# Kernel tuning notes

Hardware: AMD Instinct MI355X
Metric: run time of the kernel (lower is better)

## Reference

```python
import jax, jax.numpy as jnp
import numpy as np

HEADS = 8
K = 3            # kernel_size per axis
RPB = 2 * K - 1  # rel-pos-bias extent per axis
EPS = 1e-5


def _nbr(dim, k):
    # NATTEN-style clamped window: shift window to stay fully inside [0, dim)
    q = jnp.arange(dim)
    start = jnp.clip(q - k // 2, 0, dim - k)
    nbr = start[:, None] + jnp.arange(k)[None, :]       # (dim, k) neighbor coords
    rel = nbr - q[:, None] + (k - 1)                    # (dim, k) in [0, 2k-2]
    return nbr, rel


def _instance_norm(x):
    # InstanceNorm3d, affine=False: normalize over spatial dims per (B, C)
    m = jnp.mean(x, axis=(2, 3, 4), keepdims=True)
    v = jnp.var(x, axis=(2, 3, 4), keepdims=True)
    return (x - m) * jax.lax.rsqrt(v + EPS)


def setup_inputs() -> dict:
    key = jax.random.key(0)
    ks = jax.random.split(key, 10)
    B, C, H, W, Z = 1, 128, 32, 32, 32
    Cf = 4 * C
    s = 0.02
    return {
        "x": jax.random.normal(ks[0], (B, C, H, W, Z), jnp.float32),
        "w_qkv": jax.random.normal(ks[1], (3 * C, C), jnp.float32) * s,
        "b_qkv": jnp.zeros((3 * C,), jnp.float32),
        "rpb": jax.random.normal(ks[2], (HEADS, RPB, RPB, RPB), jnp.float32) * s,
        "w_proj": jax.random.normal(ks[3], (C, C), jnp.float32) * s,
        "b_proj": jnp.zeros((C,), jnp.float32),
        "w_ffn1": jax.random.normal(ks[4], (Cf, C), jnp.float32) * s,
        "b_ffn1": jnp.zeros((Cf,), jnp.float32),
        "w_ffn2": jax.random.normal(ks[5], (C, Cf), jnp.float32) * s,
        "b_ffn2": jnp.zeros((C,), jnp.float32),
    }


def reference(x, w_qkv, b_qkv, rpb, w_proj, b_proj, w_ffn1, b_ffn1, w_ffn2, b_ffn2):
    B, C, H, W, Z = x.shape
    hd = C // HEADS
    N = H * W * Z
    KK = K ** 3

    # ---- SAM: 3D neighborhood self-attention ----
    xt = x.reshape(B, C, N).transpose(0, 2, 1)                 # (B, N, C)
    qkv = xt @ w_qkv.T + b_qkv                                  # (B, N, 3C)
    q, k_, v = jnp.split(qkv, 3, axis=-1)
    split = lambda t: t.reshape(B, N, HEADS, hd).transpose(0, 2, 1, 3)  # (B, h, N, d)
    q, k_, v = split(q), split(k_), split(v)

    nh, rh = _nbr(H, K)
    nw, rw = _nbr(W, K)
    nz, rz = _nbr(Z, K)
    # flat neighbor token index per (h, w, z, kh, kw, kz)
    nbr = ((nh[:, None, None, :, None, None] * W
            + nw[None, :, None, None, :, None]) * Z
           + nz[None, None, :, None, None, :]).reshape(N, KK)   # (N, 27)
    # flat rel-pos-bias index
    bidx = ((rh[:, None, None, :, None, None] * RPB
             + rw[None, :, None, None, :, None]) * RPB
            + rz[None, None, :, None, None, :]).reshape(N, KK)  # (N, 27)

    kg = k_[:, :, nbr]                                          # (B, h, N, 27, d)
    vg = v[:, :, nbr]                                           # (B, h, N, 27, d)
    bias = rpb.reshape(HEADS, RPB ** 3)[:, bidx]                # (h, N, 27)

    scale = jnp.asarray(hd, x.dtype) ** -0.5
    attn = jnp.einsum('bhnd,bhnkd->bhnk', q * scale, kg) + bias
    attn = jax.nn.softmax(attn, axis=-1)
    out = jnp.einsum('bhnk,bhnkd->bhnd', attn, vg)              # (B, h, N, d)
    out = out.transpose(0, 2, 1, 3).reshape(B, N, C) @ w_proj.T + b_proj
    x5 = out.transpose(0, 2, 1).reshape(B, C, H, W, Z)

    # ---- norm_in ----
    x5 = _instance_norm(x5)

    # ---- FFN (mmcv-style, GELU, residual identity) ----
    t = x5.reshape(B, C, N).transpose(0, 2, 1)                  # (B, N, C)
    t = t + (jax.nn.gelu(t @ w_ffn1.T + b_ffn1) @ w_ffn2.T + b_ffn2)
    x5 = t.transpose(0, 2, 1).reshape(B, C, H, W, Z)

    # ---- norm_out ----
    return _instance_norm(x5)
```

## Files before the change

kernel.cpp:

```cpp
#include <hip/hip_runtime.h>
#include <hip/hip_bf16.h>
#include <math.h>

#define NPOS 32768
#define CCH  128
#define C3   384
#define CF   512

typedef __attribute__((ext_vector_type(8))) short short8;
typedef __attribute__((ext_vector_type(4))) float f32x4;

__device__ inline float bf2f(unsigned short u) {
    union { unsigned int i; float f; } x; x.i = ((unsigned int)u) << 16; return x.f;
}
__device__ inline unsigned short f2bf(float f) {
    union { float f; unsigned int i; } x; x.f = f;
    unsigned int r = x.i + 0x7FFFu + ((x.i >> 16) & 1u);
    return (unsigned short)(r >> 16);
}
__device__ inline float lo_bf(unsigned int u) {
    union { unsigned int i; float f; } x; x.i = u << 16; return x.f;
}
__device__ inline float hi_bf(unsigned int u) {
    union { unsigned int i; float f; } x; x.i = u & 0xffff0000u; return x.f;
}

template<bool GELU, bool RES, bool WF32, bool WBF>
__global__ __launch_bounds__(256) void gemm_mfma(
    const unsigned short* __restrict__ A, const unsigned short* __restrict__ B,
    const float* __restrict__ bias, const unsigned short* __restrict__ res,
    float* __restrict__ outf, unsigned short* __restrict__ outb,
    int M, int Nout, int K)
{
    __shared__ alignas(16) unsigned short As[128 * 40];
    __shared__ alignas(16) unsigned short Bs[128 * 40];

    const int tid  = threadIdx.x;
    const int lane = tid & 63;
    const int wave = tid >> 6;
    const int wm = wave & 1, wn = wave >> 1;
    const int row0 = blockIdx.y * 128;
    const int col0 = blockIdx.x * 128;

    const f32x4 fzero = {0.f, 0.f, 0.f, 0.f};
    f32x4 acc[4][4];
    #pragma unroll
    for (int i = 0; i < 4; ++i)
        #pragma unroll
        for (int j = 0; j < 4; ++j) acc[i][j] = fzero;

    const int lr = lane & 15;
    const int lk = (lane >> 4) * 8;

    for (int kt = 0; kt < K; kt += 32) {
        #pragma unroll
        for (int it = 0; it < 2; ++it) {
            const int c = tid + it * 256;
            const int r = c >> 2;
            const int p = (c & 3) * 8;
            *(uint4*)&As[r * 40 + p] = *(const uint4*)&A[(size_t)(row0 + r) * K + kt + p];
            *(uint4*)&Bs[r * 40 + p] = *(const uint4*)&B[(size_t)(col0 + r) * K + kt + p];
        }
        __syncthreads();
        short8 af[4], bfr[4];
        #pragma unroll
        for (int i = 0; i < 4; ++i)
            af[i]  = *(const short8*)&As[(wm * 64 + i * 16 + lr) * 40 + lk];
        #pragma unroll
        for (int j = 0; j < 4; ++j)
            bfr[j] = *(const short8*)&Bs[(wn * 64 + j * 16 + lr) * 40 + lk];
        #pragma unroll
        for (int i = 0; i < 4; ++i)
            #pragma unroll
            for (int j = 0; j < 4; ++j)
                acc[i][j] = __builtin_amdgcn_mfma_f32_16x16x32_bf16(
                                af[i], bfr[j], acc[i][j], 0, 0, 0);
        __syncthreads();
    }

    const int gr0 = row0 + wm * 64 + (lane >> 4) * 4;
    const int gc0 = col0 + wn * 64 + lr;
    #pragma unroll
    for (int j = 0; j < 4; ++j) {
        const int gc = gc0 + j * 16;
        const float bv = bias[gc];
        #pragma unroll
        for (int i = 0; i < 4; ++i) {
            #pragma unroll
            for (int r = 0; r < 4; ++r) {
                const int gr = gr0 + i * 16 + r;
                float v = acc[i][j][r] + bv;
                if (GELU) {
                    const float g = 0.7978845608028654f * (v + 0.044715f * v * v * v);
                    const float e = __expf(2.f * g);
                    v = v * (e / (e + 1.f));
                }
                if (RES)  v += bf2f(res[(size_t)gr * Nout + gc]);
                if (WF32) outf[(size_t)gr * Nout + gc] = v;
                if (WBF)  outb[(size_t)gr * Nout + gc] = f2bf(v);
            }
        }
    }
}

__global__ __launch_bounds__(256) void attn_tiled(
    const unsigned short* __restrict__ qkv, const float* __restrict__ rpb,
    unsigned short* __restrict__ out)
{
    __shared__ unsigned int ksu[288 * 8];
    __shared__ unsigned int vsu[288 * 8];
    __shared__ unsigned int qsu[32 * 8];
    __shared__ float logits[32 * 29];
    __shared__ float rpbs[125];

    const int t  = threadIdx.x;
    const int line = ((blockIdx.x & 7) << 7) + (blockIdx.x >> 3);
    const int h  = blockIdx.y;
    const int w0 = line & 31, h0 = line >> 5;
    const int n0 = (h0 << 10) + (w0 << 5);
    const int sh0 = min(max(h0 - 1, 0), 29);
    const int sw0 = min(max(w0 - 1, 0), 29);
    const int rh_off = sh0 - h0 + 2;
    const int rw_off = sw0 - w0 + 2;

    if (t < 64) {
        const int pos = t >> 1, part = t & 1;
        const uint4 raw = *(const uint4*)&qkv[(size_t)(n0 + pos) * C3 + h * 16 + part * 8];
        *(uint4*)&qsu[pos * 8 + part * 4] = raw;
    } else if (t < 192) {
        const int i = t - 64;
        if (i < 125) rpbs[i] = rpb[h * 125 + i];
    }
    for (int c = t; c < 1152; c += 256) {
        const int p = c >> 2, part = c & 3;
        const int ihw = p >> 5, z = p & 31;
        const int ih = (ihw * 11) >> 5;
        const int iw = ihw - 3 * ih;
        const int n = ((sh0 + ih) << 10) + ((sw0 + iw) << 5) + z;
        const uint4 raw = *(const uint4*)&qkv[(size_t)n * C3 + CCH + (part >> 1) * CCH
                                              + h * 16 + (part & 1) * 8];
        unsigned int* d = ((part < 2) ? ksu : vsu) + p * 8 + (part & 1) * 4;
        *(uint4*)d = raw;
    }
    __syncthreads();

    {
        const int q = t >> 3, j = t & 7;
        const int sz = min(max(q - 1, 0), 29);
        const int rz_off = sz - q + 2;
        float qf[16];
        #pragma unroll
        for (int d2 = 0; d2 < 8; ++d2) {
            const unsigned int u = qsu[q * 8 + d2];
            qf[2 * d2] = lo_bf(u); qf[2 * d2 + 1] = hi_bf(u);
        }
        for (int kk = j; kk < 27; kk += 8) {
            const int ihw = kk / 3, dz = kk - 3 * ihw;
            const int ih = ihw / 3,  iw = ihw - 3 * ih;
            const int p = ihw * 32 + sz + dz;
            float a = 0.f;
            #pragma unroll
            for (int d2 = 0; d2 < 8; ++d2) {
                const unsigned int u = ksu[p * 8 + d2];
                a += qf[2 * d2] * lo_bf(u) + qf[2 * d2 + 1] * hi_bf(u);
            }
            const int bidx = ((ih + rh_off) * 5 + (iw + rw_off)) * 5 + (dz + rz_off);
            logits[q * 29 + kk] = a * 0.25f + rpbs[bidx];
        }
    }
    __syncthreads();

    if (t < 32) {
        float mx = -1e30f;
        #pragma unroll
        for (int kk = 0; kk < 27; ++kk) mx = fmaxf(mx, logits[t * 29 + kk]);
        float s = 0.f;
        #pragma unroll
        for (int kk = 0; kk < 27; ++kk) {
            const float e = __expf(logits[t * 29 + kk] - mx);
            logits[t * 29 + kk] = e; s += e;
        }
        const float inv = 1.f / s;
        #pragma unroll
        for (int kk = 0; kk < 27; ++kk) logits[t * 29 + kk] *= inv;
    }
    __syncthreads();

    {
        const int q = t >> 3, d2 = t & 7;
        const int sz = min(max(q - 1, 0), 29);
        float ax = 0.f, ay = 0.f;
        #pragma unroll
        for (int kk = 0; kk < 27; ++kk) {
            const int p = (kk / 3) * 32 + sz + (kk % 3);
            const float w = logits[q * 29 + kk];
            const unsigned int u = vsu[p * 8 + d2];
            ax += w * lo_bf(u); ay += w * hi_bf(u);
        }
        const unsigned int o = ((unsigned int)f2bf(ay) << 16) | (unsigned int)f2bf(ax);
        *(unsigned int*)&out[(size_t)(n0 + q) * CCH + h * 16 + d2 * 2] = o;
    }
}

__global__ __launch_bounds__(128) void stats_kernel(
    const float* __restrict__ a, float* __restrict__ stats)
{
    const int c = threadIdx.x;
    const int r0 = blockIdx.x * 128;
    float s = 0.f, sq = 0.f;
    for (int r = 0; r < 128; ++r) {
        const float v = a[(size_t)(r0 + r) * CCH + c];
        s += v; sq += v * v;
    }
    atomicAdd(&stats[c], s);
    atomicAdd(&stats[CCH + c], sq);
}

__global__ __launch_bounds__(256) void prep_kernel(
    const float* __restrict__ wq, const float* __restrict__ wp,
    const float* __restrict__ w1, const float* __restrict__ w2,
    unsigned short* __restrict__ wq_b, unsigned short* __restrict__ wp_b,
    unsigned short* __restrict__ w1_b, unsigned short* __restrict__ w2_b,
    float* __restrict__ stats)
{
    const int i = blockIdx.x * 256 + threadIdx.x;
    if (blockIdx.x == 0) {
        stats[threadIdx.x] = 0.f;
        stats[threadIdx.x + 256] = 0.f;
    }
    const float* src; unsigned short* dst; int off;
    if (i < 12288)      { src = wq; dst = wq_b; off = i; }
    else if (i < 16384) { src = wp; dst = wp_b; off = i - 12288; }
    else if (i < 32768) { src = w1; dst = w1_b; off = i - 16384; }
    else                { src = w2; dst = w2_b; off = i - 32768; }
    const float4 v = ((const float4*)src)[off];
    ushort4 o;
    o.x = f2bf(v.x); o.y = f2bf(v.y); o.z = f2bf(v.z); o.w = f2bf(v.w);
    ((ushort4*)dst)[off] = o;
}

__global__ __launch_bounds__(256) void norm_apply_bf(
    const float* __restrict__ a, const float* __restrict__ stats,
    unsigned short* __restrict__ o)
{
    const int i = blockIdx.x * 256 + threadIdx.x;
    const int c0 = (i * 4) & (CCH - 1);
    const float4 v = ((const float4*)a)[i];
    const float invN = 1.f / (float)NPOS;
    ushort4 r;
    #pragma unroll
    for (int j = 0; j < 4; ++j) {
        const int c = c0 + j;
        const float m = stats[c] * invN;
        const float var = stats[CCH + c] * invN - m * m;
        const float rs = rsqrtf(var + 1e-5f);
        (&r.x)[j] = f2bf(((&v.x)[j] - m) * rs);
    }
    *(ushort4*)&o[(size_t)i * 4] = r;
}

__global__ void norm_transpose_kernel(
    const float* __restrict__ t, const float* __restrict__ stats,
    float* __restrict__ out)
{
    __shared__ float tile[32][33];
    const int n0 = blockIdx.x * 32;
    const int c0 = blockIdx.y * 32;
    const int tx = threadIdx.x;
    const int ty = threadIdx.y;
    for (int i = ty; i < 32; i += 8)
        tile[i][tx] = t[(size_t)(n0 + i) * CCH + c0 + tx];
    __syncthreads();
    const float invN = 1.f / (float)NPOS;
    for (int i = ty; i < 32; i += 8) {
        const int c = c0 + i;
        const float m = stats[c] * invN;
        const float var = stats[CCH + c] * invN - m * m;
        const float rs = rsqrtf(var + 1e-5f);
        out[(size_t)c * NPOS + n0 + tx] = (tile[tx][i] - m) * rs;
    }
}

__global__ __launch_bounds__(256) void transpose_x_kernel(
    const float* __restrict__ x, unsigned short* __restrict__ xt)
{
    __shared__ float tile[32][33];
    const int n0 = blockIdx.x * 32;
    const int c0 = blockIdx.y * 32;
    const int tx = threadIdx.x & 31;
    const int ty = threadIdx.x >> 5;
    for (int i = ty; i < 32; i += 8)
        tile[i][tx] = x[(size_t)(c0 + i) * NPOS + n0 + tx];
    __syncthreads();
    for (int i = ty; i < 32; i += 8)
        xt[(size_t)(n0 + i) * CCH + c0 + tx] = f2bf(tile[tx][i]);
}

extern "C" void kernel_launch(void* const* d_in, const int* in_sizes, int n_in,
                              void* d_out, int out_size, void* d_ws, size_t ws_size,
                              hipStream_t stream)
{
    const float* x      = (const float*)d_in[0];
    const float* w_qkv  = (const float*)d_in[1];
    const float* b_qkv  = (const float*)d_in[2];
    const float* rpb    = (const float*)d_in[3];
    const float* w_proj = (const float*)d_in[4];
    const float* b_proj = (const float*)d_in[5];
    const float* w_ffn1 = (const float*)d_in[6];
    const float* b_ffn1 = (const float*)d_in[7];
    const float* w_ffn2 = (const float*)d_in[8];
    const float* b_ffn2 = (const float*)d_in[9];
    float* out = (float*)d_out;

    char* ws = (char*)d_ws;
    unsigned short* xt_bf    = (unsigned short*)(ws + 0);
    unsigned short* qkv_bf   = (unsigned short*)(ws + 8388608);
    unsigned short* ffn1_bf  = (unsigned short*)(ws + 0);
    unsigned short* attnO_bf = (unsigned short*)(ws + 33554432);
    float*          x5       = (float*)(ws + 41943040);
    unsigned short* x5n_bf   = (unsigned short*)(ws + 58720256);
    float*          tbuf     = (float*)(ws + 67108864);
    unsigned short* wqkv_bf  = (unsigned short*)(ws + 83886080);
    unsigned short* wproj_bf = (unsigned short*)(ws + 83984384);
    unsigned short* wffn1_bf = (unsigned short*)(ws + 84017152);
    unsigned short* wffn2_bf = (unsigned short*)(ws + 84148224);
    float*          stats    = (float*)(ws + 84279296);

    prep_kernel<<<192, 256, 0, stream>>>(w_qkv, w_proj, w_ffn1, w_ffn2,
                                         wqkv_bf, wproj_bf, wffn1_bf, wffn2_bf, stats);
    transpose_x_kernel<<<dim3(NPOS / 32, CCH / 32), 256, 0, stream>>>(x, xt_bf);

    gemm_mfma<false, false, false, true><<<dim3(C3 / 128, NPOS / 128), 256, 0, stream>>>(
        xt_bf, wqkv_bf, b_qkv, nullptr, nullptr, qkv_bf, NPOS, C3, CCH);

    attn_tiled<<<dim3(1024, 8), 256, 0, stream>>>(qkv_bf, rpb, attnO_bf);

    gemm_mfma<false, false, true, false><<<dim3(1, NPOS / 128), 256, 0, stream>>>(
        attnO_bf, wproj_bf, b_proj, nullptr, x5, nullptr, NPOS, CCH, CCH);

    stats_kernel<<<256, 128, 0, stream>>>(x5, stats);
    norm_apply_bf<<<(NPOS * CCH / 4) / 256, 256, 0, stream>>>(x5, stats, x5n_bf);

    gemm_mfma<true, false, false, true><<<dim3(CF / 128, NPOS / 128), 256, 0, stream>>>(
        x5n_bf, wffn1_bf, b_ffn1, nullptr, nullptr, ffn1_bf, NPOS, CF, CCH);

    gemm_mfma<false, true, true, false><<<dim3(1, NPOS / 128), 256, 0, stream>>>(
        ffn1_bf, wffn2_bf, b_ffn2, x5n_bf, tbuf, nullptr, NPOS, CCH, CF);

    stats_kernel<<<256, 128, 0, stream>>>(tbuf, stats + 256);
    norm_transpose_kernel<<<dim3(NPOS / 32, CCH / 32), dim3(32, 8), 0, stream>>>(
        tbuf, stats + 256, out);
}
```

Measured before the change: 212.7 us.

## Fuse instance-norm apply into FFN GEMMs, narrow N tiles, vectorize stats and epilogue

Removes the separate norm_apply kernel and x5n bf16 buffer. The FFN1 GEMM now normalizes the fp32 x5 on the fly while loading its A tile, and the FFN2 GEMM recomputes the normalized residual from x5 in its epilogue. Both CCH-wide GEMMs use 64-column tiles to double their block count. The MFMA operands are swapped so each lane holds 4 consecutive columns, which allows float4/ushort4 vectorized stores. The stats kernel is rewritten with float4 loads and an LDS reduction, at the cost of more blocks issuing atomics and extra fp32 reads in the GEMM loaders.

```diff
diff --git a/kernel.cpp b/kernel.cpp
--- a/kernel.cpp
+++ b/kernel.cpp
@@ -25,79 +25,133 @@
     union { unsigned int i; float f; } x; x.i = u & 0xffff0000u; return x.f;
 }
 
-template<bool GELU, bool RES, bool WF32, bool WBF>
+template<int NJ, bool NORMA, bool GELU, bool NORMRES, bool WF32, bool WBF>
 __global__ __launch_bounds__(256) void gemm_mfma(
-    const unsigned short* __restrict__ A, const unsigned short* __restrict__ B,
-    const float* __restrict__ bias, const unsigned short* __restrict__ res,
+    const unsigned short* __restrict__ Abf, const float* __restrict__ Af32,
+    const unsigned short* __restrict__ B,
+    const float* __restrict__ bias, const float* __restrict__ resf,
+    const float* __restrict__ stats,
     float* __restrict__ outf, unsigned short* __restrict__ outb,
     int M, int Nout, int K)
 {
+    constexpr int NT = NJ * 32;
+    constexpr int NT2 = NT / 2;
     __shared__ alignas(16) unsigned short As[128 * 40];
-    __shared__ alignas(16) unsigned short Bs[128 * 40];
+    __shared__ alignas(16) unsigned short Bs[NT * 40];
+    __shared__ alignas(16) float mLDS[128];
+    __shared__ alignas(16) float rsLDS[128];
 
     const int tid  = threadIdx.x;
     const int lane = tid & 63;
     const int wave = tid >> 6;
     const int wm = wave & 1, wn = wave >> 1;
     const int row0 = blockIdx.y * 128;
-    const int col0 = blockIdx.x * 128;
+    const int col0 = blockIdx.x * NT;
+
+    if (NORMA || NORMRES) {
+        if (tid < 128) {
+            const float invN = 1.f / (float)NPOS;
+            const float m = stats[tid] * invN;
+            const float var = stats[128 + tid] * invN - m * m;
+            mLDS[tid] = m;
+            rsLDS[tid] = rsqrtf(var + 1e-5f);
+        }
+        __syncthreads();
+    }
 
     const f32x4 fzero = {0.f, 0.f, 0.f, 0.f};
-    f32x4 acc[4][4];
+    f32x4 acc[4][NJ];
     #pragma unroll
     for (int i = 0; i < 4; ++i)
         #pragma unroll
-        for (int j = 0; j < 4; ++j) acc[i][j] = fzero;
+        for (int j = 0; j < NJ; ++j) acc[i][j] = fzero;
 
     const int lr = lane & 15;
-    const int lk = (lane >> 4) * 8;
+    const int quad = lane >> 4;
+    const int lk = quad * 8;
 
     for (int kt = 0; kt < K; kt += 32) {
-        #pragma unroll
-        for (int it = 0; it < 2; ++it) {
-            const int c = tid + it * 256;
+        for (int c = tid; c < (128 + NT) * 4; c += 256) {
             const int r = c >> 2;
             const int p = (c & 3) * 8;
-            *(uint4*)&As[r * 40 + p] = *(const uint4*)&A[(size_t)(row0 + r) * K + kt + p];
-            *(uint4*)&Bs[r * 40 + p] = *(const uint4*)&B[(size_t)(col0 + r) * K + kt + p];
+            if (r < 128) {
+                if (NORMA) {
+                    const float4 v0 = *(const float4*)&Af32[(size_t)(row0 + r) * K + kt + p];
+                    const float4 v1 = *(const float4*)&Af32[(size_t)(row0 + r) * K + kt + p + 4];
+                    ushort4 o0, o1;
+                    #pragma unroll
+                    for (int e = 0; e < 4; ++e) {
+                        const int c0 = kt + p + e, c1 = kt + p + 4 + e;
+                        (&o0.x)[e] = f2bf(((&v0.x)[e] - mLDS[c0]) * rsLDS[c0]);
+                        (&o1.x)[e] = f2bf(((&v1.x)[e] - mLDS[c1]) * rsLDS[c1]);
+                    }
+                    *(ushort4*)&As[r * 40 + p]     = o0;
+                    *(ushort4*)&As[r * 40 + p + 4] = o1;
+                } else {
+                    *(uint4*)&As[r * 40 + p] =
+                        *(const uint4*)&Abf[(size_t)(row0 + r) * K + kt + p];
+                }
+            } else {
+                const int rb = r - 128;
+                *(uint4*)&Bs[rb * 40 + p] =
+                    *(const uint4*)&B[(size_t)(col0 + rb) * K + kt + p];
+            }
         }
         __syncthreads();
-        short8 af[4], bfr[4];
+        short8 af[4], bfr[NJ];
         #pragma unroll
         for (int i = 0; i < 4; ++i)
             af[i]  = *(const short8*)&As[(wm * 64 + i * 16 + lr) * 40 + lk];
         #pragma unroll
-        for (int j = 0; j < 4; ++j)
-            bfr[j] = *(const short8*)&Bs[(wn * 64 + j * 16 + lr) * 40 + lk];
+        for (int j = 0; j < NJ; ++j)
+            bfr[j] = *(const short8*)&Bs[(wn * NT2 + j * 16 + lr) * 40 + lk];
         #pragma unroll
         for (int i = 0; i < 4; ++i)
             #pragma unroll
-            for (int j = 0; j < 4; ++j)
+            for (int j = 0; j < NJ; ++j)
                 acc[i][j] = __builtin_amdgcn_mfma_f32_16x16x32_bf16(
-                                af[i], bfr[j], acc[i][j], 0, 0, 0);
+                                bfr[j], af[i], acc[i][j], 0, 0, 0);
         __syncthreads();
     }
 
-    const int gr0 = row0 + wm * 64 + (lane >> 4) * 4;
-    const int gc0 = col0 + wn * 64 + lr;
+    float4 bias4[NJ];
     #pragma unroll
-    for (int j = 0; j < 4; ++j) {
-        const int gc = gc0 + j * 16;
-        const float bv = bias[gc];
-        #pragma unroll
-        for (int i = 0; i < 4; ++i) {
+    for (int j = 0; j < NJ; ++j)
+        bias4[j] = *(const float4*)&bias[col0 + wn * NT2 + j * 16 + quad * 4];
+
+    #pragma unroll
+    for (int i = 0; i < 4; ++i) {
+        const int m = row0 + wm * 64 + i * 16 + lr;
+        #pragma unroll
+        for (int j = 0; j < NJ; ++j) {
+            const int n0 = col0 + wn * NT2 + j * 16 + quad * 4;
+            float v[4];
             #pragma unroll
             for (int r = 0; r < 4; ++r) {
-                const int gr = gr0 + i * 16 + r;
-                float v = acc[i][j][r] + bv;
+                v[r] = acc[i][j][r] + (&bias4[j].x)[r];
                 if (GELU) {
-                    const float g = 0.7978845608028654f * (v + 0.044715f * v * v * v);
+                    const float g = 0.7978845608028654f *
+                        (v[r] + 0.044715f * v[r] * v[r] * v[r]);
                     const float e = __expf(2.f * g);
-                    v = v * (e / (e + 1.f));
+                    v[r] = v[r] * (e / (e + 1.f));
                 }
-                if (RES)  v += bf2f(res[(size_t)gr * Nout + gc]);
-                if (WF32) outf[(size_t)gr * Nout + gc] = v;
-                if (WBF)  outb[(size_t)gr * Nout + gc] = f2bf(v);
+            }
+            if (NORMRES) {
+                const float4 rv = *(const float4*)&resf[(size_t)m * Nout + n0];
+                const float4 mm = *(const float4*)&mLDS[n0];
+                const float4 rs = *(const float4*)&rsLDS[n0];
+                #pragma unroll
+                for (int r = 0; r < 4; ++r)
+                    v[r] += ((&rv.x)[r] - (&mm.x)[r]) * (&rs.x)[r];
+            }
+            if (WF32) {
+                float4 o; o.x = v[0]; o.y = v[1]; o.z = v[2]; o.w = v[3];
+                *(float4*)&outf[(size_t)m * Nout + n0] = o;
+            }
+            if (WBF) {
+                ushort4 o;
+                o.x = f2bf(v[0]); o.y = f2bf(v[1]); o.z = f2bf(v[2]); o.w = f2bf(v[3]);
+                *(ushort4*)&outb[(size_t)m * Nout + n0] = o;
             }
         }
     }
@@ -202,18 +256,49 @@
     }
 }
 
-__global__ __launch_bounds__(128) void stats_kernel(
+__global__ __launch_bounds__(256) void stats_v2(
     const float* __restrict__ a, float* __restrict__ stats)
 {
-    const int c = threadIdx.x;
-    const int r0 = blockIdx.x * 128;
-    float s = 0.f, sq = 0.f;
-    for (int r = 0; r < 128; ++r) {
-        const float v = a[(size_t)(r0 + r) * CCH + c];
-        s += v; sq += v * v;
-    }
-    atomicAdd(&stats[c], s);
-    atomicAdd(&stats[CCH + c], sq);
+    __shared__ float4 redS[8][32];
+    __shared__ float4 redQ[8][32];
+    const int tid = threadIdx.x;
+    const int c4 = tid & 31;
+    const int r  = tid >> 5;
+    const int r0 = blockIdx.x * 64;
+
+    float4 s = {0.f, 0.f, 0.f, 0.f}, q = {0.f, 0.f, 0.f, 0.f};
+    #pragma unroll
+    for (int k = 0; k < 8; ++k) {
+        const float4 v = *(const float4*)&a[(size_t)(r0 + r * 8 + k) * CCH + c4 * 4];
+        s.x += v.x; s.y += v.y; s.z += v.z; s.w += v.w;
+        q.x += v.x * v.x; q.y += v.y * v.y; q.z += v.z * v.z; q.w += v.w * v.w;
+    }
+    redS[r][c4] = s; redQ[r][c4] = q;
+    __syncthreads();
+    if (tid < 32) {
+        float4 t = redS[0][tid];
+        #pragma unroll
+        for (int k = 1; k < 8; ++k) {
+            const float4 v = redS[k][tid];
+            t.x += v.x; t.y += v.y; t.z += v.z; t.w += v.w;
+        }
+        atomicAdd(&stats[tid * 4 + 0], t.x);
+        atomicAdd(&stats[tid * 4 + 1], t.y);
+        atomicAdd(&stats[tid * 4 + 2], t.z);
+        atomicAdd(&stats[tid * 4 + 3], t.w);
+    } else if (tid < 64) {
+        const int c = tid - 32;
+        float4 t = redQ[0][c];
+        #pragma unroll
+        for (int k = 1; k < 8; ++k) {
+            const float4 v = redQ[k][c];
+            t.x += v.x; t.y += v.y; t.z += v.z; t.w += v.w;
+        }
+        atomicAdd(&stats[CCH + c * 4 + 0], t.x);
+        atomicAdd(&stats[CCH + c * 4 + 1], t.y);
+        atomicAdd(&stats[CCH + c * 4 + 2], t.z);
+        atomicAdd(&stats[CCH + c * 4 + 3], t.w);
+    }
 }
 
 __global__ __launch_bounds__(256) void prep_kernel(
@@ -237,26 +322,6 @@
     ushort4 o;
     o.x = f2bf(v.x); o.y = f2bf(v.y); o.z = f2bf(v.z); o.w = f2bf(v.w);
     ((ushort4*)dst)[off] = o;
-}
-
-__global__ __launch_bounds__(256) void norm_apply_bf(
-    const float* __restrict__ a, const float* __restrict__ stats,
-    unsigned short* __restrict__ o)
-{
-    const int i = blockIdx.x * 256 + threadIdx.x;
-    const int c0 = (i * 4) & (CCH - 1);
-    const float4 v = ((const float4*)a)[i];
-    const float invN = 1.f / (float)NPOS;
-    ushort4 r;
-    #pragma unroll
-    for (int j = 0; j < 4; ++j) {
-        const int c = c0 + j;
-        const float m = stats[c] * invN;
-        const float var = stats[CCH + c] * invN - m * m;
-        const float rs = rsqrtf(var + 1e-5f);
-        (&r.x)[j] = f2bf(((&v.x)[j] - m) * rs);
-    }
-    *(ushort4*)&o[(size_t)i * 4] = r;
 }
 
 __global__ void norm_transpose_kernel(
@@ -318,36 +383,44 @@
     unsigned short* ffn1_bf  = (unsigned short*)(ws + 0);
     unsigned short* attnO_bf = (unsigned short*)(ws + 33554432);
     float*          x5       = (float*)(ws + 41943040);
-    unsigned short* x5n_bf   = (unsigned short*)(ws + 58720256);
     float*          tbuf     = (float*)(ws + 67108864);
     unsigned short* wqkv_bf  = (unsigned short*)(ws + 83886080);
     unsigned short* wproj_bf = (unsigned short*)(ws + 83984384);
     unsigned short* wffn1_bf = (unsigned short*)(ws + 84017152);
     unsigned short* wffn2_bf = (unsigned short*)(ws + 84148224);
     float*          stats    = (float*)(ws + 84279296);
+    float* stats1 = stats;
+    float* stats2 = stats + 256;
 
     prep_kernel<<<192, 256, 0, stream>>>(w_qkv, w_proj, w_ffn1, w_ffn2,
                                          wqkv_bf, wproj_bf, wffn1_bf, wffn2_bf, stats);
     transpose_x_kernel<<<dim3(NPOS / 32, CCH / 32), 256, 0, stream>>>(x, xt_bf);
 
-    gemm_mfma<false, false, false, true><<<dim3(C3 / 128, NPOS / 128), 256, 0, stream>>>(
-        xt_bf, wqkv_bf, b_qkv, nullptr, nullptr, qkv_bf, NPOS, C3, CCH);
+    gemm_mfma<4, false, false, false, false, true>
+        <<<dim3(C3 / 128, NPOS / 128), 256, 0, stream>>>(
+        xt_bf, nullptr, wqkv_bf, b_qkv, nullptr, nullptr,
+        nullptr, qkv_bf, NPOS, C3, CCH);
 
     attn_tiled<<<dim3(1024, 8), 256, 0, stream>>>(qkv_bf, rpb, attnO_bf);
 
-    gemm_mfma<false, false, true, false><<<dim3(1, NPOS / 128), 256, 0, stream>>>(
-        attnO_bf, wproj_bf, b_proj, nullptr, x5, nullptr, NPOS, CCH, CCH);
-
-    stats_kernel<<<256, 128, 0, stream>>>(x5, stats);
-    norm_apply_bf<<<(NPOS * CCH / 4) / 256, 256, 0, stream>>>(x5, stats, x5n_bf);
-
-    gemm_mfma<true, false, false, true><<<dim3(CF / 128, NPOS / 128), 256, 0, stream>>>(
-        x5n_bf, wffn1_bf, b_ffn1, nullptr, nullptr, ffn1_bf, NPOS, CF, CCH);
-
-    gemm_mfma<false, true, true, false><<<dim3(1, NPOS / 128), 256, 0, stream>>>(
-        ffn1_bf, wffn2_bf, b_ffn2, x5n_bf, tbuf, nullptr, NPOS, CCH, CF);
-
-    stats_kernel<<<256, 128, 0, stream>>>(tbuf, stats + 256);
+    gemm_mfma<2, false, false, false, true, false>
+        <<<dim3(CCH / 64, NPOS / 128), 256, 0, stream>>>(
+        attnO_bf, nullptr, wproj_bf, b_proj, nullptr, nullptr,
+        x5, nullptr, NPOS, CCH, CCH);
+
+    stats_v2<<<NPOS / 64, 256, 0, stream>>>(x5, stats1);
+
+    gemm_mfma<4, true, true, false, false, true>
+        <<<dim3(CF / 128, NPOS / 128), 256, 0, stream>>>(
+        nullptr, x5, wffn1_bf, b_ffn1, nullptr, stats1,
+        nullptr, ffn1_bf, NPOS, CF, CCH);
+
+    gemm_mfma<2, false, false, true, true, false>
+        <<<dim3(CCH / 64, NPOS / 128), 256, 0, stream>>>(
+        ffn1_bf, nullptr, wffn2_bf, b_ffn2, x5, stats1,
+        tbuf, nullptr, NPOS, CCH, CF);
+
+    stats_v2<<<NPOS / 64, 256, 0, stream>>>(tbuf, stats2);
     norm_transpose_kernel<<<dim3(NPOS / 32, CCH / 32), dim3(32, 8), 0, stream>>>(
-        tbuf, stats + 256, out);
-}
+        tbuf, stats2, out);
+}
```

Result: slower. 326.0 us (+53.3%).
